# Kernel optimization log

Measured on AMD Instinct MI355X. Metric: run time of the kernel, lower is better.

The kernel has to match this reference:

```python
import jax, jax.numpy as jnp
import numpy as np
import math

B, S, E, H = 2, 2048, 1024, 16
D = E // H  # head_size = 64
EPS = 1e-5

def _ln(x, g, b):
    mu = jnp.mean(x, axis=-1, keepdims=True)
    var = jnp.mean(jnp.square(x - mu), axis=-1, keepdims=True)
    return (x - mu) * jax.lax.rsqrt(var + EPS) * g + b

def setup_inputs() -> dict:
    key = jax.random.key(0)
    ks = jax.random.split(key, 16)
    s = 0.02
    return {
        "I": jax.random.normal(ks[0], (B, S, E), jnp.float32),
        "x": jax.random.normal(ks[1], (B, S, E), jnp.float32),
        "mask": jnp.ones((B, 1, S), jnp.int32),
        # per-head Q/K/V weights stacked over heads [H, E, D], biases [H, D]
        "wq": jax.random.normal(ks[2], (H, E, D), jnp.float32) * s,
        "bq": jax.random.normal(ks[3], (H, D), jnp.float32) * s,
        "wk": jax.random.normal(ks[4], (H, E, D), jnp.float32) * s,
        "bk": jax.random.normal(ks[5], (H, D), jnp.float32) * s,
        "wv": jax.random.normal(ks[6], (H, E, D), jnp.float32) * s,
        "bv": jax.random.normal(ks[7], (H, D), jnp.float32) * s,
        "w_proj": jax.random.normal(ks[8], (E, E), jnp.float32) * s,
        "b_proj": jnp.zeros((E,), jnp.float32),
        "g1": jnp.ones((E,), jnp.float32),
        "be1": jnp.zeros((E,), jnp.float32),
        "g2": jnp.ones((E,), jnp.float32),
        "be2": jnp.zeros((E,), jnp.float32),
        "w1": jax.random.normal(ks[9], (E, 4 * E), jnp.float32) * s,
        "b1": jnp.zeros((4 * E,), jnp.float32),
        "w2": jax.random.normal(ks[10], (4 * E, E), jnp.float32) * s,
        "b2": jnp.zeros((E,), jnp.float32),
    }

def reference(I, x, mask, wq, bq, wk, bk, wv, bv, w_proj, b_proj,
              g1, be1, g2, be2, w1, b1, w2, b2):
    xn = _ln(x, g1, be1)
    # batched per-head projections: [B,S,E] x [H,E,D] -> [B,H,S,D]
    q = jnp.einsum('bse,hed->bhsd', I, wq) + bq[None, :, None, :]
    k = jnp.einsum('bse,hed->bhsd', xn, wk) + bk[None, :, None, :]
    v = jnp.einsum('bse,hed->bhsd', xn, wv) + bv[None, :, None, :]
    # NOTE: original scales by sqrt(n_embed), not sqrt(head_size)
    scores = jnp.einsum('bhqd,bhkd->bhqk', q, k) / math.sqrt(E)
    scores = jnp.where(mask[:, None, :, :] == 0, -1e9, scores)
    attn = jax.nn.softmax(scores, axis=-1)
    ctx = jnp.einsum('bhqk,bhkd->bhqd', attn, v)
    # concat heads: [B,S,H,D] -> [B,S,E]
    ctx = ctx.transpose(0, 2, 1, 3).reshape(B, S, E)
    attn_out = ctx @ w_proj + b_proj
    h = xn + attn_out
    h2 = _ln(h, g2, be2)
    ff = jax.nn.gelu(h2 @ w1 + b1, approximate=False) @ w2 + b2
    return h2 + ff
```

## Files before the change

### kernel.cpp

```cpp
#include <hip/hip_runtime.h>
#include <hip/hip_bf16.h>
#include <math.h>

typedef short short8 __attribute__((ext_vector_type(8)));
typedef short short4_t __attribute__((ext_vector_type(4)));
typedef float f32x4 __attribute__((ext_vector_type(4)));
typedef unsigned short u16;
typedef unsigned int u32;

#define B_ 2
#define S_ 2048
#define E_ 1024
#define H_ 16
#define D_ 64
#define TOK (B_*S_)

__device__ __forceinline__ float bf2f(u16 u) {
    union { unsigned int u; float f; } v; v.u = ((unsigned int)u) << 16; return v.f;
}
__device__ __forceinline__ u16 f2bf(float f) {
    union { float f; unsigned int u; } v; v.f = f;
    unsigned int r = v.u + 0x7fffu + ((v.u >> 16) & 1u);
    return (u16)(r >> 16);
}
__device__ __forceinline__ u32 fbits(float f) {
    union { float f; u32 u; } v; v.f = f; return v.u;
}
__device__ __forceinline__ void gl_lds16(const u16* g, short* l) {
    __builtin_amdgcn_global_load_lds(
        (const __attribute__((address_space(1))) unsigned int*)(g),
        (__attribute__((address_space(3))) unsigned int*)(l), 16, 0, 0);
}

__global__ __launch_bounds__(256) void convf_k(const float* __restrict__ s, u16* __restrict__ d)
{
    size_t i = ((size_t)blockIdx.x * 256 + threadIdx.x) * 8;
    f32x4 a = *(const f32x4*)(s + i);
    f32x4 b = *(const f32x4*)(s + i + 4);
    short8 r;
#pragma unroll
    for (int j = 0; j < 4; j++) { r[j] = (short)f2bf(a[j]); r[4 + j] = (short)f2bf(b[j]); }
    *(short8*)(d + i) = r;
}

__global__ __launch_bounds__(256) void tconv_k(
    const float* __restrict__ src, u16* __restrict__ dst,
    int K, int N, size_t zsrc, size_t zdst)
{
    __shared__ u16 t[64][72];
    src += (size_t)blockIdx.z * zsrc;
    dst += (size_t)blockIdx.z * zdst;
    int k0 = blockIdx.y * 64, n0 = blockIdx.x * 64;
    int tid = threadIdx.x;
    int kr = tid >> 4, nc = (tid & 15) * 4;
#pragma unroll
    for (int i = 0; i < 4; i++) {
        f32x4 v = *(const f32x4*)(src + (size_t)(k0 + kr + i * 16) * N + n0 + nc);
#pragma unroll
        for (int j = 0; j < 4; j++) t[kr + i * 16][nc + j] = f2bf(v[j]);
    }
    __syncthreads();
    int nr = tid >> 2, kg = (tid & 3) * 16;
    short8 r0, r1;
#pragma unroll
    for (int j = 0; j < 8; j++) { r0[j] = (short)t[kg + j][nr]; r1[j] = (short)t[kg + 8 + j][nr]; }
    u16* dp = dst + (size_t)(n0 + nr) * K + k0 + kg;
    *(short8*)(dp) = r0;
    *(short8*)(dp + 8) = r1;
}

__global__ __launch_bounds__(256) void tconvqkv_k(
    const float* __restrict__ wq, const float* __restrict__ wk,
    const float* __restrict__ wv, u16* __restrict__ dst)
{
    __shared__ u16 t[64][72];
    int z = blockIdx.z;
    int w = z >> 4, hh = z & 15;
    const float* src = (w == 0 ? wq : (w == 1 ? wk : wv)) + (size_t)hh * E_ * D_;
    u16* d = dst + (size_t)w * E_ * E_ + (size_t)hh * D_ * E_;
    int k0 = blockIdx.y * 64;
    int tid = threadIdx.x;
    int kr = tid >> 4, nc = (tid & 15) * 4;
#pragma unroll
    for (int i = 0; i < 4; i++) {
        f32x4 v = *(const f32x4*)(src + (size_t)(k0 + kr + i * 16) * D_ + nc);
#pragma unroll
        for (int j = 0; j < 4; j++) t[kr + i * 16][nc + j] = f2bf(v[j]);
    }
    __syncthreads();
    int nr = tid >> 2, kg = (tid & 3) * 16;
    short8 r0, r1;
#pragma unroll
    for (int j = 0; j < 8; j++) { r0[j] = (short)t[kg + j][nr]; r1[j] = (short)t[kg + 8 + j][nr]; }
    u16* dp = d + (size_t)nr * E_ + k0 + kg;
    *(short8*)(dp) = r0;
    *(short8*)(dp + 8) = r1;
}

__global__ __launch_bounds__(256) void vtrans_k(const u16* __restrict__ V, u16* __restrict__ Vt)
{
    __shared__ u16 t[64][72];
    int s0 = blockIdx.x * 64, h = blockIdx.y, b = blockIdx.z;
    int tid = threadIdx.x;
    int sr = tid >> 2, dc = (tid & 3) * 16;
    const u16* src = V + (size_t)b * S_ * E_ + (size_t)(s0 + sr) * E_ + h * D_ + dc;
    short8 v0 = *(const short8*)(src);
    short8 v1 = *(const short8*)(src + 8);
#pragma unroll
    for (int j = 0; j < 8; j++) { t[sr][dc + j] = v0[j]; t[sr][dc + 8 + j] = v1[j]; }
    __syncthreads();
    int dr = tid >> 2, sc = (tid & 3) * 16;
    short8 r0, r1;
#pragma unroll
    for (int j = 0; j < 8; j++) { r0[j] = (short)t[sc + j][dr]; r1[j] = (short)t[sc + 8 + j][dr]; }
    u16* dp = Vt + ((size_t)(b * H_ + h) * D_ + dr) * S_ + s0 + sc;
    *(short8*)(dp) = r0;
    *(short8*)(dp + 8) = r1;
}

__global__ __launch_bounds__(256) void maskprep_k(
    const int* __restrict__ mask, float* __restrict__ fb, int* __restrict__ ok)
{
    __shared__ unsigned char fl[256];
    int b = blockIdx.x;
    int tid = threadIdx.x;
    int base = tid * 8;
    unsigned all = 1;
#pragma unroll
    for (int j = 0; j < 8; j++) {
        int m = mask[b * S_ + base + j];
        fb[b * S_ + base + j] = m ? 0.f : -1e9f;
        all &= (m != 0) ? 1u : 0u;
    }
    fl[tid] = (unsigned char)all;
    __syncthreads();
    if (tid < 32) {
        unsigned a = 1;
#pragma unroll
        for (int j = 0; j < 8; j++) a &= fl[tid * 8 + j];
        ok[b * 32 + tid] = (int)a;
    }
}

template<int INF32>
__global__ __launch_bounds__(256) void ln_kernel(
    const void* __restrict__ xv, const float* __restrict__ g,
    const float* __restrict__ be, u16* __restrict__ y)
{
    int lane = threadIdx.x & 63, wave = threadIdx.x >> 6;
    int row = blockIdx.x * 4 + wave;
    int c0 = lane * 16;
    float v[16];
    if (INF32) {
        const float* xr = (const float*)xv + (size_t)row * E_ + c0;
#pragma unroll
        for (int i = 0; i < 4; i++) {
            f32x4 xx = *(const f32x4*)(xr + i * 4);
#pragma unroll
            for (int j = 0; j < 4; j++) v[i * 4 + j] = xx[j];
        }
    } else {
        const u16* xr = (const u16*)xv + (size_t)row * E_ + c0;
        short8 a = *(const short8*)(xr);
        short8 b = *(const short8*)(xr + 8);
#pragma unroll
        for (int j = 0; j < 8; j++) { v[j] = bf2f((u16)a[j]); v[8 + j] = bf2f((u16)b[j]); }
    }
    float s = 0.f, q = 0.f;
#pragma unroll
    for (int i = 0; i < 16; i++) { s += v[i]; q += v[i] * v[i]; }
#pragma unroll
    for (int off = 1; off < 64; off <<= 1) {
        s += __shfl_xor(s, off, 64);
        q += __shfl_xor(q, off, 64);
    }
    float mu = s * (1.0f / E_);
    float var = q * (1.0f / E_) - mu * mu;
    float rstd = rsqrtf(var + 1e-5f);
    u16* yr = y + (size_t)row * E_ + c0;
    short8 o0, o1;
#pragma unroll
    for (int j = 0; j < 8; j++) {
        o0[j] = (short)f2bf((v[j] - mu) * rstd * g[c0 + j] + be[c0 + j]);
        o1[j] = (short)f2bf((v[8 + j] - mu) * rstd * g[c0 + 8 + j] + be[c0 + 8 + j]);
    }
    *(short8*)(yr) = o0;
    *(short8*)(yr + 8) = o1;
}

template<int GELU, int RES, int CF32, int QKV>
__global__ __launch_bounds__(256) void gemm2_k(
    const u16* __restrict__ A, const u16* __restrict__ Axn,
    const u16* __restrict__ WT,
    const float* __restrict__ bq, const float* __restrict__ bk, const float* __restrict__ bv,
    const u16* __restrict__ res, void* __restrict__ Cv, int M, int N, int K)
{
    __shared__ __align__(16) short a_sh[2][128 * 32];
    __shared__ __align__(16) short b_sh[2][128 * 32];
    int tid = threadIdx.x;
    int wave = tid >> 6, lane = tid & 63, quad = lane >> 4, l16 = lane & 15;
    int wm = wave >> 1, wn = wave & 1;
    int m0 = blockIdx.y * 128, n0 = blockIdx.x * 128;

    int which = QKV ? (n0 >> 10) : 0;
    const u16* Ause = (QKV && which) ? Axn : A;
    const float* bias = QKV ? (which == 0 ? bq : (which == 1 ? bk : bv)) : bq;

    f32x4 acc[4][4];
#pragma unroll
    for (int mt = 0; mt < 4; mt++)
#pragma unroll
        for (int nt = 0; nt < 4; nt++)
            acc[mt][nt] = (f32x4){0.f, 0.f, 0.f, 0.f};

    int srow = lane >> 2;
    int c = ((lane & 3) ^ ((lane >> 3) & 3)) * 8;
    const u16* Ab = Ause + (size_t)(m0 + wave * 32 + srow) * K + c;
    const u16* Bb = WT + (size_t)(n0 + wave * 32 + srow) * K + c;
    short* al0 = &a_sh[0][wave * 1024];
    short* al1 = &a_sh[1][wave * 1024];
    short* bl0 = &b_sh[0][wave * 1024];
    short* bl1 = &b_sh[1][wave * 1024];
    int xo = (quad ^ ((l16 >> 1) & 3)) * 8;

    for (int kk = 0; kk < K; kk += 64) {
        __syncthreads();
        gl_lds16(Ab + kk, al0);
        gl_lds16(Ab + kk + (size_t)16 * K, al0 + 512);
        gl_lds16(Ab + kk + 32, al1);
        gl_lds16(Ab + kk + (size_t)16 * K + 32, al1 + 512);
        gl_lds16(Bb + kk, bl0);
        gl_lds16(Bb + kk + (size_t)16 * K, bl0 + 512);
        gl_lds16(Bb + kk + 32, bl1);
        gl_lds16(Bb + kk + (size_t)16 * K + 32, bl1 + 512);
        __syncthreads();

#pragma unroll
        for (int h = 0; h < 2; h++) {
            short8 af[4], bf8[4];
#pragma unroll
            for (int mt = 0; mt < 4; mt++)
                af[mt] = *(const short8*)(&a_sh[h][(wm * 64 + mt * 16 + l16) * 32 + xo]);
#pragma unroll
            for (int nt = 0; nt < 4; nt++)
                bf8[nt] = *(const short8*)(&b_sh[h][(wn * 64 + nt * 16 + l16) * 32 + xo]);
#pragma unroll
            for (int mt = 0; mt < 4; mt++)
#pragma unroll
                for (int nt = 0; nt < 4; nt++)
                    acc[mt][nt] = __builtin_amdgcn_mfma_f32_16x16x32_bf16(af[mt], bf8[nt], acc[mt][nt], 0, 0, 0);
        }
    }

    int ostride = QKV ? 1024 : N;
    u16* C16 = QKV ? ((u16*)Cv + (size_t)which * (size_t)M * 1024) : (u16*)Cv;
#pragma unroll
    for (int mt = 0; mt < 4; mt++) {
#pragma unroll
        for (int nt = 0; nt < 4; nt++) {
            int ng = n0 + wn * 64 + nt * 16 + l16;
            int col = QKV ? (ng & 1023) : ng;
            float bb = bias[col];
#pragma unroll
            for (int r = 0; r < 4; r++) {
                int row = m0 + wm * 64 + mt * 16 + quad * 4 + r;
                float v = acc[mt][nt][r] + bb;
                if (QKV && which == 0) v *= 0.03125f;
                if (RES) v += bf2f(res[(size_t)row * ostride + col]);
                if (GELU) v = 0.5f * v * (1.0f + erff(v * 0.70710678118f));
                if (CF32) ((float*)Cv)[(size_t)row * ostride + col] = v;
                else C16[(size_t)row * ostride + col] = f2bf(v);
            }
        }
    }
}

__global__ __launch_bounds__(256) void gemmsk_k(
    const u16* __restrict__ A, const u16* __restrict__ WT,
    u16* __restrict__ P, int M, int N, int K, int Ks)
{
    __shared__ __align__(16) short a_sh[2][128 * 32];
    __shared__ __align__(16) short b_sh[2][128 * 32];
    int tid = threadIdx.x;
    int wave = tid >> 6, lane = tid & 63, quad = lane >> 4, l16 = lane & 15;
    int wm = wave >> 1, wn = wave & 1;
    int m0 = blockIdx.y * 128, n0 = blockIdx.x * 128;
    int koff = blockIdx.z * Ks;

    f32x4 acc[4][4];
#pragma unroll
    for (int mt = 0; mt < 4; mt++)
#pragma unroll
        for (int nt = 0; nt < 4; nt++)
            acc[mt][nt] = (f32x4){0.f, 0.f, 0.f, 0.f};

    int srow = lane >> 2;
    int c = ((lane & 3) ^ ((lane >> 3) & 3)) * 8;
    const u16* Ab = A + (size_t)(m0 + wave * 32 + srow) * K + koff + c;
    const u16* Bb = WT + (size_t)(n0 + wave * 32 + srow) * K + koff + c;
    short* al0 = &a_sh[0][wave * 1024];
    short* al1 = &a_sh[1][wave * 1024];
    short* bl0 = &b_sh[0][wave * 1024];
    short* bl1 = &b_sh[1][wave * 1024];
    int xo = (quad ^ ((l16 >> 1) & 3)) * 8;

    for (int kk = 0; kk < Ks; kk += 64) {
        __syncthreads();
        gl_lds16(Ab + kk, al0);
        gl_lds16(Ab + kk + (size_t)16 * K, al0 + 512);
        gl_lds16(Ab + kk + 32, al1);
        gl_lds16(Ab + kk + (size_t)16 * K + 32, al1 + 512);
        gl_lds16(Bb + kk, bl0);
        gl_lds16(Bb + kk + (size_t)16 * K, bl0 + 512);
        gl_lds16(Bb + kk + 32, bl1);
        gl_lds16(Bb + kk + (size_t)16 * K + 32, bl1 + 512);
        __syncthreads();

#pragma unroll
        for (int h = 0; h < 2; h++) {
            short8 af[4], bf8[4];
#pragma unroll
            for (int mt = 0; mt < 4; mt++)
                af[mt] = *(const short8*)(&a_sh[h][(wm * 64 + mt * 16 + l16) * 32 + xo]);
#pragma unroll
            for (int nt = 0; nt < 4; nt++)
                bf8[nt] = *(const short8*)(&b_sh[h][(wn * 64 + nt * 16 + l16) * 32 + xo]);
#pragma unroll
            for (int mt = 0; mt < 4; mt++)
#pragma unroll
                for (int nt = 0; nt < 4; nt++)
                    acc[mt][nt] = __builtin_amdgcn_mfma_f32_16x16x32_bf16(af[mt], bf8[nt], acc[mt][nt], 0, 0, 0);
        }
    }

    u16* Pz = P + (size_t)blockIdx.z * (size_t)M * N;
#pragma unroll
    for (int mt = 0; mt < 4; mt++) {
#pragma unroll
        for (int nt = 0; nt < 4; nt++) {
            int col = n0 + wn * 64 + nt * 16 + l16;
#pragma unroll
            for (int r = 0; r < 4; r++) {
                int row = m0 + wm * 64 + mt * 16 + quad * 4 + r;
                Pz[(size_t)row * N + col] = f2bf(acc[mt][nt][r]);
            }
        }
    }
}

__global__ __launch_bounds__(256) void combine2_k(
    const u16* __restrict__ P, const float* __restrict__ bias,
    const u16* __restrict__ res, float* __restrict__ out)
{
    const size_t MN = (size_t)TOK * E_;
    size_t i = ((size_t)blockIdx.x * 256 + threadIdx.x) * 8;
    int col = (int)(i & (E_ - 1));
    float v[8];
    f32x4 b0 = *(const f32x4*)(bias + col);
    f32x4 b1 = *(const f32x4*)(bias + col + 4);
    short8 rr = *(const short8*)(res + i);
#pragma unroll
    for (int j = 0; j < 4; j++) { v[j] = b0[j] + bf2f((u16)rr[j]); v[4 + j] = b1[j] + bf2f((u16)rr[4 + j]); }
#pragma unroll
    for (int z = 0; z < 2; z++) {
        short8 p = *(const short8*)(P + z * MN + i);
#pragma unroll
        for (int j = 0; j < 8; j++) v[j] += bf2f((u16)p[j]);
    }
    f32x4 o0, o1;
#pragma unroll
    for (int j = 0; j < 4; j++) { o0[j] = v[j]; o1[j] = v[4 + j]; }
    *(f32x4*)(out + i) = o0;
    *(f32x4*)(out + i + 4) = o1;
}

template<int GELU, int RES, int CF32>
__global__ __launch_bounds__(256) void gemm3_k(
    const u16* __restrict__ A, const u16* __restrict__ WT,
    const float* __restrict__ bias, const u16* __restrict__ res,
    void* __restrict__ Cv, int M, int N, int K)
{
    __shared__ __align__(16) short a_sh[2][128 * 32];
    __shared__ __align__(16) short b_sh[2][64 * 32];
    int tid = threadIdx.x;
    int wave = tid >> 6, lane = tid & 63, quad = lane >> 4, l16 = lane & 15;
    int wm = wave >> 1, wn = wave & 1;
    int m0 = blockIdx.y * 128, n0 = blockIdx.x * 64;

    f32x4 acc[4][2];
#pragma unroll
    for (int mt = 0; mt < 4; mt++)
#pragma unroll
        for (int nt = 0; nt < 2; nt++)
            acc[mt][nt] = (f32x4){0.f, 0.f, 0.f, 0.f};

    int srow = lane >> 2;
    int c = ((lane & 3) ^ ((lane >> 3) & 3)) * 8;
    const u16* Ab = A + (size_t)(m0 + wave * 32 + srow) * K + c;
    const u16* Bb = WT + (size_t)(n0 + wave * 16 + srow) * K + c;
    short* al0 = &a_sh[0][wave * 1024];
    short* al1 = &a_sh[1][wave * 1024];
    short* bl0 = &b_sh[0][wave * 512];
    short* bl1 = &b_sh[1][wave * 512];
    int xo = (quad ^ ((l16 >> 1) & 3)) * 8;

    for (int kk = 0; kk < K; kk += 64) {
        __syncthreads();
        gl_lds16(Ab + kk, al0);
        gl_lds16(Ab + kk + (size_t)16 * K, al0 + 512);
        gl_lds16(Ab + kk + 32, al1);
        gl_lds16(Ab + kk + (size_t)16 * K + 32, al1 + 512);
        gl_lds16(Bb + kk, bl0);
        gl_lds16(Bb + kk + 32, bl1);
        __syncthreads();

#pragma unroll
        for (int h = 0; h < 2; h++) {
            short8 af[4], bf8[2];
#pragma unroll
            for (int mt = 0; mt < 4; mt++)
                af[mt] = *(const short8*)(&a_sh[h][(wm * 64 + mt * 16 + l16) * 32 + xo]);
#pragma unroll
            for (int nt = 0; nt < 2; nt++)
                bf8[nt] = *(const short8*)(&b_sh[h][(wn * 32 + nt * 16 + l16) * 32 + xo]);
#pragma unroll
            for (int mt = 0; mt < 4; mt++)
#pragma unroll
                for (int nt = 0; nt < 2; nt++)
                    acc[mt][nt] = __builtin_amdgcn_mfma_f32_16x16x32_bf16(af[mt], bf8[nt], acc[mt][nt], 0, 0, 0);
        }
    }

#pragma unroll
    for (int mt = 0; mt < 4; mt++) {
#pragma unroll
        for (int nt = 0; nt < 2; nt++) {
            int col = n0 + wn * 32 + nt * 16 + l16;
            float bb = bias[col];
#pragma unroll
            for (int r = 0; r < 4; r++) {
                int row = m0 + wm * 64 + mt * 16 + quad * 4 + r;
                float v = acc[mt][nt][r] + bb;
                if (RES) v += bf2f(res[(size_t)row * N + col]);
                if (GELU) v = 0.5f * v * (1.0f + erff(v * 0.70710678118f));
                if (CF32) ((float*)Cv)[(size_t)row * N + col] = v;
                else ((u16*)Cv)[(size_t)row * N + col] = f2bf(v);
            }
        }
    }
}

__global__ __launch_bounds__(512) void attn_k(
    const u16* __restrict__ Q, const u16* __restrict__ K,
    const u16* __restrict__ Vt, const float* __restrict__ fb,
    const int* __restrict__ ok, u16* __restrict__ O)
{
    __shared__ __align__(16) short k_sh[2][2][64 * 32];
    __shared__ __align__(16) short v_sh[2][2][64 * 32];
    __shared__ __align__(16) short p_sh[8][16 * 72];
    int tid = threadIdx.x;
    int wave = tid >> 6, lane = tid & 63, quad = lane >> 4, l16 = lane & 15;
    int qb = blockIdx.x, h = blockIdx.y, b = blockIdx.z;
    int q0 = qb * 128;
    const u16* Qp = Q + (size_t)b * S_ * E_ + (size_t)h * D_;
    const u16* Kp = K + (size_t)b * S_ * E_ + (size_t)h * D_;
    const u16* Vtp = Vt + (size_t)(b * H_ + h) * D_ * S_;

    int qrow = q0 + wave * 16 + l16;
    short8 qf0 = *(const short8*)(Qp + (size_t)qrow * E_ + quad * 8);
    short8 qf1 = *(const short8*)(Qp + (size_t)qrow * E_ + 32 + quad * 8);

    f32x4 o[4];
#pragma unroll
    for (int dt = 0; dt < 4; dt++) o[dt] = (f32x4){0.f, 0.f, 0.f, 0.f};
    float rs_tot = 0.f;

    int sub = wave & 1, rblk = wave >> 1;
    int srow = lane >> 2;
    int c = ((lane & 3) ^ ((lane >> 3) & 3)) * 8;
    const u16* Kg = Kp + (size_t)(rblk * 16 + srow) * E_ + sub * 32 + c;
    const u16* Vg = Vtp + (size_t)(rblk * 16 + srow) * S_ + sub * 32 + c;
    short* kl0 = &k_sh[0][sub][rblk * 512];
    short* kl1 = &k_sh[1][sub][rblk * 512];
    short* vl0 = &v_sh[0][sub][rblk * 512];
    short* vl1 = &v_sh[1][sub][rblk * 512];

    gl_lds16(Kg, kl0);
    gl_lds16(Vg, vl0);
    __syncthreads();

    const float* fbb = fb + b * S_;
    const int* okb = ok + b * 32;
    int xo = (quad ^ ((l16 >> 1) & 3)) * 8;

    for (int kt = 0; kt < S_ / 64; kt++) {
        int cur = kt & 1;
        if (kt < 31) {
            gl_lds16(Kg + (size_t)(kt + 1) * 64 * E_, cur ? kl0 : kl1);
            gl_lds16(Vg + (kt + 1) * 64, cur ? vl0 : vl1);
        }

        f32x4 s[4];
#pragma unroll
        for (int mt = 0; mt < 4; mt++) {
            int ro = (mt * 16 + l16) * 32 + xo;
            short8 kf0 = *(const short8*)(&k_sh[cur][0][ro]);
            short8 kf1 = *(const short8*)(&k_sh[cur][1][ro]);
            s[mt] = __builtin_amdgcn_mfma_f32_16x16x32_bf16(kf0, qf0, (f32x4){0.f,0.f,0.f,0.f}, 0, 0, 0);
            s[mt] = __builtin_amdgcn_mfma_f32_16x16x32_bf16(kf1, qf1, s[mt], 0, 0, 0);
        }

        if (!okb[kt]) {
#pragma unroll
            for (int mt = 0; mt < 4; mt++)
#pragma unroll
                for (int r = 0; r < 4; r++)
                    s[mt][r] += fbb[kt * 64 + mt * 16 + quad * 4 + r];
        }

#pragma unroll
        for (int mt = 0; mt < 4; mt++) {
            float p0 = __expf(s[mt][0]);
            float p1 = __expf(s[mt][1]);
            float p2 = __expf(s[mt][2]);
            float p3 = __expf(s[mt][3]);
            rs_tot += (p0 + p1) + (p2 + p3);
            u32 u0 = __builtin_amdgcn_perm(fbits(p1), fbits(p0), 0x07060302u);
            u32 u1 = __builtin_amdgcn_perm(fbits(p3), fbits(p2), 0x07060302u);
            uint2 pk; pk.x = u0; pk.y = u1;
            *(uint2*)(&p_sh[wave][l16 * 72 + mt * 16 + quad * 4]) = pk;
        }

#pragma unroll
        for (int sk = 0; sk < 2; sk++) {
            short8 pf = *(const short8*)(&p_sh[wave][l16 * 72 + sk * 32 + quad * 8]);
#pragma unroll
            for (int dt = 0; dt < 4; dt++) {
                short8 vf = *(const short8*)(&v_sh[cur][sk][(dt * 16 + l16) * 32 + xo]);
                o[dt] = __builtin_amdgcn_mfma_f32_16x16x32_bf16(vf, pf, o[dt], 0, 0, 0);
            }
        }
        __syncthreads();
    }

    rs_tot += __shfl_xor(rs_tot, 16, 64);
    rs_tot += __shfl_xor(rs_tot, 32, 64);
    float inv = 1.0f / rs_tot;
    u16* Op = O + (size_t)b * S_ * E_ + (size_t)(q0 + wave * 16 + l16) * E_ + h * D_;
#pragma unroll
    for (int dt = 0; dt < 4; dt++) {
        short4_t pk;
#pragma unroll
        for (int r = 0; r < 4; r++) pk[r] = (short)f2bf(o[dt][r] * inv);
        *(short4_t*)(Op + dt * 16 + quad * 4) = pk;
    }
}

extern "C" void kernel_launch(void* const* d_in, const int* in_sizes, int n_in,
                              void* d_out, int out_size, void* d_ws, size_t ws_size,
                              hipStream_t stream)
{
    (void)in_sizes; (void)n_in; (void)out_size; (void)ws_size;
    const float* I      = (const float*)d_in[0];
    const float* x      = (const float*)d_in[1];
    const int*   mask   = (const int*)d_in[2];
    const float* wq     = (const float*)d_in[3];
    const float* bq     = (const float*)d_in[4];
    const float* wk     = (const float*)d_in[5];
    const float* bk     = (const float*)d_in[6];
    const float* wv     = (const float*)d_in[7];
    const float* bv     = (const float*)d_in[8];
    const float* w_proj = (const float*)d_in[9];
    const float* b_proj = (const float*)d_in[10];
    const float* g1     = (const float*)d_in[11];
    const float* be1    = (const float*)d_in[12];
    const float* g2     = (const float*)d_in[13];
    const float* be2    = (const float*)d_in[14];
    const float* w1     = (const float*)d_in[15];
    const float* b1     = (const float*)d_in[16];
    const float* w2     = (const float*)d_in[17];
    const float* b2     = (const float*)d_in[18];
    float* out = (float*)d_out;

    char* ws = (char*)d_ws;
    const size_t SZ = (size_t)TOK * E_;
    u16* xn   = (u16*)(ws);
    u16* qb_  = (u16*)(ws + SZ * 2);
    u16* kb_  = (u16*)(ws + SZ * 4);
    u16* vb_  = (u16*)(ws + SZ * 6);
    u16* Vt   = (u16*)(ws + SZ * 8);
    u16* Ibf  = (u16*)(ws + SZ * 8);
    u16* ctx  = (u16*)(ws + SZ * 6);
    u16* hb   = (u16*)(ws + SZ * 4);
    u16* h2   = (u16*)(ws);
    u16* a1   = (u16*)(ws + SZ * 2);
    u16* WTqkv  = (u16*)(ws + 40u * 1024 * 1024);
    u16* WTproj = (u16*)(ws + 46u * 1024 * 1024);
    u16* WT1    = (u16*)(ws + 48u * 1024 * 1024);
    u16* WT2    = (u16*)(ws + 56u * 1024 * 1024);
    u16* Pp     = (u16*)(ws + 40u * 1024 * 1024);
    float* fbm  = (float*)(ws + 40u * 1024 * 1024);
    int*   okm  = (int*)(ws + 40u * 1024 * 1024 + 16384);

    convf_k<<<dim3(TOK * E_ / (256 * 8)), 256, 0, stream>>>(I, Ibf);
    tconvqkv_k<<<dim3(1, 16, 48), 256, 0, stream>>>(wq, wk, wv, WTqkv);
    tconv_k<<<dim3(16, 16, 1), 256, 0, stream>>>(w_proj, WTproj, E_, E_, 0, 0);
    tconv_k<<<dim3(64, 16, 1), 256, 0, stream>>>(w1, WT1, E_, 4 * E_, 0, 0);
    tconv_k<<<dim3(16, 64, 1), 256, 0, stream>>>(w2, WT2, 4 * E_, E_, 0, 0);

    ln_kernel<1><<<TOK / 4, 256, 0, stream>>>(x, g1, be1, xn);

    gemm2_k<0,0,0,1><<<dim3(24, TOK / 128), 256, 0, stream>>>(
        Ibf, xn, WTqkv, bq, bk, bv, nullptr, qb_, TOK, 1024, E_);

    maskprep_k<<<dim3(B_), 256, 0, stream>>>(mask, fbm, okm);
    vtrans_k<<<dim3(S_ / 64, H_, B_), 256, 0, stream>>>(vb_, Vt);

    attn_k<<<dim3(S_ / 128, H_, B_), 512, 0, stream>>>(qb_, kb_, Vt, fbm, okm, ctx);

    gemm3_k<0,1,0><<<dim3(16, TOK / 128), 256, 0, stream>>>(
        ctx, WTproj, b_proj, xn, hb, TOK, E_, E_);
    ln_kernel<0><<<TOK / 4, 256, 0, stream>>>(hb, g2, be2, h2);
    gemm2_k<1,0,0,0><<<dim3(32, TOK / 128), 256, 0, stream>>>(
        h2, nullptr, WT1, b1, nullptr, nullptr, nullptr, a1, TOK, 4 * E_, E_);
    gemmsk_k<<<dim3(8, TOK / 128, 2), 256, 0, stream>>>(
        a1, WT2, Pp, TOK, E_, 4 * E_, 2 * E_);
    combine2_k<<<dim3(TOK * E_ / (256 * 8)), 256, 0, stream>>>(Pp, b2, h2, out);
}
```

Measured before the change: 404.6 us.

## Replace 128x128 GEMM with 256x256 8-wave pipelined kernel for QKV and FFN1

Swaps the QKV and FFN1 GEMMs to a new kernel that uses 256x256 output tiles, 512 threads (8 waves) and K-steps of 64. Global-to-LDS loads for the next tiles are interleaved with MFMA phases using explicit barriers, waitcnt and setprio. The goal is more data reuse per LDS load and better overlap of memory with compute. The trade-offs are 128KB of LDS, a large accumulator register footprint, and far fewer blocks: 192 for QKV and 256 for FFN1, against 256 CUs on the MI355X.

New measurement: 384.7 us. -4.9%, faster.

```diff
diff --git a/kernel.cpp b/kernel.cpp
--- a/kernel.cpp
+++ b/kernel.cpp
@@ -188,91 +188,121 @@
     *(short8*)(yr + 8) = o1;
 }
 
-template<int GELU, int RES, int CF32, int QKV>
-__global__ __launch_bounds__(256) void gemm2_k(
+template<int QKV, int GELU>
+__global__ __launch_bounds__(512) void gemm8p_k(
     const u16* __restrict__ A, const u16* __restrict__ Axn,
     const u16* __restrict__ WT,
     const float* __restrict__ bq, const float* __restrict__ bk, const float* __restrict__ bv,
-    const u16* __restrict__ res, void* __restrict__ Cv, int M, int N, int K)
-{
-    __shared__ __align__(16) short a_sh[2][128 * 32];
-    __shared__ __align__(16) short b_sh[2][128 * 32];
+    u16* __restrict__ C, int M, int N, int K)
+{
+    __shared__ __align__(16) short As[2][256 * 64];
+    __shared__ __align__(16) short Bs[2][256 * 64];
     int tid = threadIdx.x;
     int wave = tid >> 6, lane = tid & 63, quad = lane >> 4, l16 = lane & 15;
-    int wm = wave >> 1, wn = wave & 1;
-    int m0 = blockIdx.y * 128, n0 = blockIdx.x * 128;
-
+    int wm = wave >> 2, wn = wave & 3;
+    int n0 = blockIdx.x * 256, m0 = blockIdx.y * 256;
     int which = QKV ? (n0 >> 10) : 0;
     const u16* Ause = (QKV && which) ? Axn : A;
     const float* bias = QKV ? (which == 0 ? bq : (which == 1 ? bk : bv)) : bq;
 
-    f32x4 acc[4][4];
-#pragma unroll
-    for (int mt = 0; mt < 4; mt++)
-#pragma unroll
-        for (int nt = 0; nt < 4; nt++)
-            acc[mt][nt] = (f32x4){0.f, 0.f, 0.f, 0.f};
-
-    int srow = lane >> 2;
-    int c = ((lane & 3) ^ ((lane >> 3) & 3)) * 8;
-    const u16* Ab = Ause + (size_t)(m0 + wave * 32 + srow) * K + c;
-    const u16* Bb = WT + (size_t)(n0 + wave * 32 + srow) * K + c;
-    short* al0 = &a_sh[0][wave * 1024];
-    short* al1 = &a_sh[1][wave * 1024];
-    short* bl0 = &b_sh[0][wave * 1024];
-    short* bl1 = &b_sh[1][wave * 1024];
-    int xo = (quad ^ ((l16 >> 1) & 3)) * 8;
-
-    for (int kk = 0; kk < K; kk += 64) {
-        __syncthreads();
-        gl_lds16(Ab + kk, al0);
-        gl_lds16(Ab + kk + (size_t)16 * K, al0 + 512);
-        gl_lds16(Ab + kk + 32, al1);
-        gl_lds16(Ab + kk + (size_t)16 * K + 32, al1 + 512);
-        gl_lds16(Bb + kk, bl0);
-        gl_lds16(Bb + kk + (size_t)16 * K, bl0 + 512);
-        gl_lds16(Bb + kk + 32, bl1);
-        gl_lds16(Bb + kk + (size_t)16 * K + 32, bl1 + 512);
-        __syncthreads();
-
-#pragma unroll
-        for (int h = 0; h < 2; h++) {
-            short8 af[4], bf8[4];
-#pragma unroll
-            for (int mt = 0; mt < 4; mt++)
-                af[mt] = *(const short8*)(&a_sh[h][(wm * 64 + mt * 16 + l16) * 32 + xo]);
-#pragma unroll
-            for (int nt = 0; nt < 4; nt++)
-                bf8[nt] = *(const short8*)(&b_sh[h][(wn * 64 + nt * 16 + l16) * 32 + xo]);
-#pragma unroll
-            for (int mt = 0; mt < 4; mt++)
-#pragma unroll
-                for (int nt = 0; nt < 4; nt++)
-                    acc[mt][nt] = __builtin_amdgcn_mfma_f32_16x16x32_bf16(af[mt], bf8[nt], acc[mt][nt], 0, 0, 0);
-        }
-    }
-
+    f32x4 acc[8][4];
+#pragma unroll
+    for (int m = 0; m < 8; m++)
+#pragma unroll
+        for (int n = 0; n < 4; n++)
+            acc[m][n] = (f32x4){0.f, 0.f, 0.f, 0.f};
+
+    int srow = lane >> 3, slot = lane & 7;
+    const u16* Ag = Ause + (size_t)(m0 + wave * 16 + srow) * K + ((slot ^ srow) << 3);
+    const u16* Bg = WT + (size_t)(n0 + wave * 16 + srow) * K + ((slot ^ srow) << 3);
+    int wv = wave * 1024;
+    int r7 = l16 & 7;
+    int soff0 = (quad ^ r7) << 3;
+    int soff1 = ((4 + quad) ^ r7) << 3;
+    int arow = (wm * 128 + l16) * 64;
+    int brow = (wn * 64 + l16) * 64;
+    int NT = K >> 6;
+
+#define GLA2(buf, h, kk_) do { \
+    gl_lds16(Ag + (size_t)((h) * 128) * K + (kk_), &As[buf][wv + (h) * 8192]); \
+    gl_lds16(Ag + (size_t)((h) * 128 + 8) * K + (kk_), &As[buf][wv + (h) * 8192 + 512]); } while (0)
+#define GLB2(buf, h, kk_) do { \
+    gl_lds16(Bg + (size_t)((h) * 128) * K + (kk_), &Bs[buf][wv + (h) * 8192]); \
+    gl_lds16(Bg + (size_t)((h) * 128 + 8) * K + (kk_), &Bs[buf][wv + (h) * 8192 + 512]); } while (0)
+
+#define PHASE(mb, GLSTMT, TAILSTMT) do { \
+    short8 af[2][2]; \
+    af[0][0] = *(const short8*)(&As[c][arow + (mb) * 1024 + soff0]); \
+    af[0][1] = *(const short8*)(&As[c][arow + (mb) * 1024 + soff1]); \
+    af[1][0] = *(const short8*)(&As[c][arow + ((mb) + 1) * 1024 + soff0]); \
+    af[1][1] = *(const short8*)(&As[c][arow + ((mb) + 1) * 1024 + soff1]); \
+    GLSTMT; \
+    __builtin_amdgcn_s_barrier(); \
+    asm volatile("s_waitcnt lgkmcnt(0)"); \
+    __builtin_amdgcn_s_setprio(1); \
+    _Pragma("unroll") \
+    for (int i_ = 0; i_ < 2; i_++) \
+    _Pragma("unroll") \
+    for (int n_ = 0; n_ < 4; n_++) { \
+        acc[(mb) + i_][n_] = __builtin_amdgcn_mfma_f32_16x16x32_bf16(af[i_][0], bf[n_][0], acc[(mb) + i_][n_], 0, 0, 0); \
+        acc[(mb) + i_][n_] = __builtin_amdgcn_mfma_f32_16x16x32_bf16(af[i_][1], bf[n_][1], acc[(mb) + i_][n_], 0, 0, 0); \
+    } \
+    __builtin_amdgcn_s_setprio(0); \
+    TAILSTMT; \
+    __builtin_amdgcn_s_barrier(); \
+} while (0)
+
+    GLB2(0, 0, 0); GLB2(0, 1, 0);
+    GLA2(0, 0, 0); GLA2(0, 1, 0);
+    if (NT > 1) {
+        GLB2(1, 0, 64); GLB2(1, 1, 64);
+        asm volatile("s_waitcnt vmcnt(4)");
+    } else {
+        asm volatile("s_waitcnt vmcnt(0)");
+    }
+    __builtin_amdgcn_s_barrier();
+
+    for (int t = 0; t < NT; ++t) {
+        int c = t & 1;
+        int kk1 = (t + 1) << 6, kk2 = (t + 2) << 6;
+        short8 bf[4][2];
+#pragma unroll
+        for (int n = 0; n < 4; n++) {
+            bf[n][0] = *(const short8*)(&Bs[c][brow + n * 1024 + soff0]);
+            bf[n][1] = *(const short8*)(&Bs[c][brow + n * 1024 + soff1]);
+        }
+        PHASE(0,
+            { if (t + 1 < NT) GLA2(c ^ 1, 0, kk1); asm volatile("s_waitcnt lgkmcnt(8)"); },
+            {});
+        PHASE(2, { if (t + 1 < NT) GLA2(c ^ 1, 1, kk1); }, {});
+        PHASE(4, { if (t + 2 < NT) GLB2(c, 0, kk2); }, {});
+        PHASE(6, { if (t + 2 < NT) GLB2(c, 1, kk2); },
+            { if (t + 2 < NT) asm volatile("s_waitcnt vmcnt(4)");
+              else            asm volatile("s_waitcnt vmcnt(0)"); });
+    }
+
+    u16* Cw = QKV ? (C + (size_t)which * (size_t)M * 1024) : C;
     int ostride = QKV ? 1024 : N;
-    u16* C16 = QKV ? ((u16*)Cv + (size_t)which * (size_t)M * 1024) : (u16*)Cv;
-#pragma unroll
-    for (int mt = 0; mt < 4; mt++) {
-#pragma unroll
-        for (int nt = 0; nt < 4; nt++) {
-            int ng = n0 + wn * 64 + nt * 16 + l16;
-            int col = QKV ? (ng & 1023) : ng;
+#pragma unroll
+    for (int m = 0; m < 8; m++) {
+#pragma unroll
+        for (int n = 0; n < 4; n++) {
+            int colg = n0 + wn * 64 + n * 16 + l16;
+            int col = QKV ? (colg & 1023) : colg;
             float bb = bias[col];
 #pragma unroll
             for (int r = 0; r < 4; r++) {
-                int row = m0 + wm * 64 + mt * 16 + quad * 4 + r;
-                float v = acc[mt][nt][r] + bb;
+                int row = m0 + wm * 128 + m * 16 + quad * 4 + r;
+                float v = acc[m][n][r] + bb;
                 if (QKV && which == 0) v *= 0.03125f;
-                if (RES) v += bf2f(res[(size_t)row * ostride + col]);
                 if (GELU) v = 0.5f * v * (1.0f + erff(v * 0.70710678118f));
-                if (CF32) ((float*)Cv)[(size_t)row * ostride + col] = v;
-                else C16[(size_t)row * ostride + col] = f2bf(v);
+                Cw[(size_t)row * ostride + col] = f2bf(v);
             }
         }
     }
+#undef GLA2
+#undef GLB2
+#undef PHASE
 }
 
 __global__ __launch_bounds__(256) void gemmsk_k(
@@ -610,8 +640,8 @@
 
     ln_kernel<1><<<TOK / 4, 256, 0, stream>>>(x, g1, be1, xn);
 
-    gemm2_k<0,0,0,1><<<dim3(24, TOK / 128), 256, 0, stream>>>(
-        Ibf, xn, WTqkv, bq, bk, bv, nullptr, qb_, TOK, 1024, E_);
+    gemm8p_k<1,0><<<dim3(12, TOK / 256), 512, 0, stream>>>(
+        Ibf, xn, WTqkv, bq, bk, bv, qb_, TOK, 3072, E_);
 
     maskprep_k<<<dim3(B_), 256, 0, stream>>>(mask, fbm, okm);
     vtrans_k<<<dim3(S_ / 64, H_, B_), 256, 0, stream>>>(vb_, Vt);
@@ -621,8 +651,8 @@
     gemm3_k<0,1,0><<<dim3(16, TOK / 128), 256, 0, stream>>>(
         ctx, WTproj, b_proj, xn, hb, TOK, E_, E_);
     ln_kernel<0><<<TOK / 4, 256, 0, stream>>>(hb, g2, be2, h2);
-    gemm2_k<1,0,0,0><<<dim3(32, TOK / 128), 256, 0, stream>>>(
-        h2, nullptr, WT1, b1, nullptr, nullptr, nullptr, a1, TOK, 4 * E_, E_);
+    gemm8p_k<0,1><<<dim3(16, TOK / 256), 512, 0, stream>>>(
+        h2, nullptr, WT1, b1, nullptr, nullptr, a1, TOK, 4 * E_, E_);
     gemmsk_k<<<dim3(8, TOK / 128, 2), 256, 0, stream>>>(
         a1, WT2, Pp, TOK, E_, 4 * E_, 2 * E_);
     combine2_k<<<dim3(TOK * E_ / (256 * 8)), 256, 0, stream>>>(Pp, b2, h2, out);
```
